# Performance work log

Measured on AMD Instinct MI355X. Metric: run time of the kernel, lower is better.

Reference implementation:

```python
import jax, jax.numpy as jnp
import numpy as np

EPS = 1e-3  # keras BatchNormalization default epsilon


def _dwconv_t(y, w):
    # depthwise conv along time (axis 1), SAME padding. y:(B,T,S,G,n), w:(G,n,k)
    k = w.shape[-1]
    T = y.shape[1]
    pl = (k - 1) // 2
    yp = jnp.pad(y, ((0, 0), (pl, k - 1 - pl), (0, 0), (0, 0), (0, 0)))
    return sum(yp[:, j:j + T] * w[..., j] for j in range(k))


def _tc_layer(x, w, b, k3, k5, k7, gamma, beta, mu, var):
    # x:(B,T,S,C); w:(5,G,Cg,nb); b/gamma/beta/mu/var:(5,G,nb); k*:(G,nb,k)
    B, T, S, C = x.shape
    G, nb = w.shape[1], w.shape[-1]
    # global spatial pooling: concat [x, max, mean] along spatial axis -> S+2
    x = jnp.concatenate([x, x.max(axis=2, keepdims=True), x.mean(axis=2, keepdims=True)], axis=2)
    S = S + 2
    xg = x.reshape(B, T, S, G, C // G)
    # 5 grouped 1x1x1 pointwise convs at once
    y = jnp.einsum('btsgc,pgcn->pbtsgn', xg, w) + b[:, None, None, None]
    t0 = y[0]
    t3 = _dwconv_t(y[1], k3)
    t5 = _dwconv_t(y[2], k5)
    t7 = _dwconv_t(y[3], k7)
    # temporal maxpool pool=2 stride=1 SAME (TF pads right)
    t1 = jnp.maximum(y[4], jnp.concatenate([y[4][:, 1:], y[4][:, -1:]], axis=1))
    ts = jnp.stack([t0, t3, t5, t7, t1])  # (5,B,T,S,G,nb)
    scale = gamma[:, None, None, None] / jnp.sqrt(var[:, None, None, None] + EPS)
    ts = (ts - mu[:, None, None, None]) * scale + beta[:, None, None, None]
    # concat branches within each group: (B,T,S,G,5*nb)
    z = jnp.transpose(ts, (1, 2, 3, 4, 0, 5)).reshape(B, T, S, G, 5 * nb)
    z = jax.nn.relu(z)
    # channel shuffle: (G, per) -> (per, G) -> flatten
    z = jnp.swapaxes(z, -1, -2).reshape(B, T, S, G * 5 * nb)
    # MaxPooling3D pool=(2,1,1) stride 2 valid: halve T
    return jnp.maximum(z[:, 0::2], z[:, 1::2])


def setup_inputs() -> dict:
    key = jax.random.key(0)
    ks = jax.random.split(key, 32)
    B, T, H, W, C = 16, 64, 7, 7, 1024
    G = 8
    d = {'x': jax.random.normal(ks[0], (B, T, H, W, C), jnp.float32)}
    specs = [(0, 128, 32), (1, 160, 40)]  # (layer, Cg, nb)
    i = 1
    for l, cg, nb in specs:
        d[f'w{l}'] = 0.02 * jax.random.normal(ks[i], (5, G, cg, nb)); i += 1
        d[f'b{l}'] = 0.02 * jax.random.normal(ks[i], (5, G, nb)); i += 1
        d[f'k3_{l}'] = 0.1 * jax.random.normal(ks[i], (G, nb, 3)); i += 1
        d[f'k5_{l}'] = 0.1 * jax.random.normal(ks[i], (G, nb, 5)); i += 1
        d[f'k7_{l}'] = 0.1 * jax.random.normal(ks[i], (G, nb, 7)); i += 1
        d[f'g{l}'] = jax.random.uniform(ks[i], (5, G, nb), minval=0.5, maxval=1.5); i += 1
        d[f'be{l}'] = 0.02 * jax.random.normal(ks[i], (5, G, nb)); i += 1
        d[f'mu{l}'] = 0.02 * jax.random.normal(ks[i], (5, G, nb)); i += 1
        d[f'v{l}'] = jax.random.uniform(ks[i], (5, G, nb), minval=0.5, maxval=1.5); i += 1
    return d


def reference(x, w0, b0, k3_0, k5_0, k7_0, g0, be0, mu0, v0,
              w1, b1, k3_1, k5_1, k7_1, g1, be1, mu1, v1):
    B, T, H, W, C = x.shape
    z = x.reshape(B, T, H * W, C)  # (B,T,S,C), side_dim2=1 kept implicit
    z = _tc_layer(z, w0, b0, k3_0, k5_0, k7_0, g0, be0, mu0, v0)
    z = _tc_layer(z, w1, b1, k3_1, k5_1, k7_1, g1, be1, mu1, v1)
    return z[:, :, :, None, :]  # (B, T/4, S+4, 1, Cout)
```

## Files before the change

### kernel.cpp

```cpp
#include <hip/hip_runtime.h>
#include <hip/hip_bf16.h>

#define EPSBN 1e-3f

typedef __attribute__((ext_vector_type(8))) short bf16x8;
typedef __attribute__((ext_vector_type(8))) unsigned short ushort8;
typedef __attribute__((ext_vector_type(4))) float f32x4;


__device__ __forceinline__ float bf2f(unsigned short u) {
    union { unsigned int i; float f; } c; c.i = (unsigned int)u << 16; return c.f;
}
__device__ __forceinline__ unsigned short f2bf(float f) {
    union { float f; unsigned int i; } c; c.f = f;
    unsigned int r = c.i + 0x7FFF + ((c.i >> 16) & 1);
    return (unsigned short)(r >> 16);
}

__global__ __launch_bounds__(256) void tc_prep(const float* __restrict__ w0,
                                               const float* __restrict__ w1,
                                               unsigned short* __restrict__ W0t,
                                               unsigned short* __restrict__ W1t) {
    const int idx = blockIdx.x * 256 + threadIdx.x;
    if (idx < 163840) {
        const int g   = idx / 20480;
        const int rem = idx - g*20480;
        const int n   = rem >> 7;
        const int k   = rem & 127;
        const int p   = n >> 5, nn = n & 31;
        W0t[idx] = f2bf(w0[(((size_t)p*8 + g)*128 + k)*32 + nn]);
    } else if (idx < 163840 + 256000) {
        const int i2  = idx - 163840;
        const int g   = i2 / 32000;
        const int rem = i2 - g*32000;
        const int n   = rem / 160;
        const int k   = rem - n*160;
        const int kref = (k % 20)*8 + k/20;
        const int p   = n / 40, nn = n - p*40;
        W1t[i2] = f2bf(w1[(((size_t)p*8 + g)*160 + kref)*40 + nn]);
    }
}

__global__ __launch_bounds__(256) void tc_reduce0(const float* __restrict__ x,
                                                  unsigned short* __restrict__ extb) {
    const int bt = blockIdx.x;
    const int b  = bt >> 6, t = bt & 63;
    const int c  = threadIdx.x * 4;
    const float4* src = reinterpret_cast<const float4*>(x + (size_t)bt * 49 * 1024 + c);
    float4 v = src[0];
    float mx0 = v.x, mx1 = v.y, mx2 = v.z, mx3 = v.w;
    float sm0 = v.x, sm1 = v.y, sm2 = v.z, sm3 = v.w;
    for (int s = 1; s < 49; ++s) {
        float4 u = src[(size_t)s * 256];
        mx0 = fmaxf(mx0, u.x); sm0 += u.x;
        mx1 = fmaxf(mx1, u.y); sm1 += u.y;
        mx2 = fmaxf(mx2, u.z); sm2 += u.z;
        mx3 = fmaxf(mx3, u.w); sm3 += u.w;
    }
    const float inv = 1.0f / 49.0f;
    ushort4 omx, omn;
    omx.x=f2bf(mx0); omx.y=f2bf(mx1); omx.z=f2bf(mx2); omx.w=f2bf(mx3);
    omn.x=f2bf(sm0*inv); omn.y=f2bf(sm1*inv); omn.z=f2bf(sm2*inv); omn.w=f2bf(sm3*inv);
    *reinterpret_cast<ushort4*>(&extb[((size_t)(b*2 + 0)*64 + t)*1024 + c]) = omx;
    *reinterpret_cast<ushort4*>(&extb[((size_t)(b*2 + 1)*64 + t)*1024 + c]) = omn;
}

__global__ __launch_bounds__(512, 4) void tc_layer0(
    const float* __restrict__ x, const unsigned short* __restrict__ extb,
    const unsigned short* __restrict__ W0t, const float* __restrict__ bias,
    const float* __restrict__ k3, const float* __restrict__ k5,
    const float* __restrict__ k7,
    const float* __restrict__ gam, const float* __restrict__ bet,
    const float* __restrict__ mu, const float* __restrict__ var,
    unsigned short* __restrict__ zb)
{
    const int tid = threadIdx.x;
    const int g   = blockIdx.x / 416;
    const int rem = blockIdx.x % 416;
    const int sp  = rem % 26;
    const int b   = rem / 26;
    const int s0  = sp*2;
    const int has1 = (s0 + 1 < 51);

    __shared__ __align__(16) unsigned short lds[128*136 + 160*40];
    unsigned short* AtU = lds;
    unsigned short* WtU = lds + 128*136;
    unsigned short* Ytb = lds;

    #pragma unroll
    for (int it = 0; it < 4; ++it) {
        const int fid = tid + it*512;
        const int row = fid >> 4;
        const int ch8 = (fid & 15) * 8;
        const int t   = row & 63;
        const int s   = (row < 64) ? s0 : (has1 ? s0+1 : s0);
        ushort8 u;
        if (s < 49) {
            const float* sp_ = x + ((size_t)(b*64 + t)*49 + s)*1024 + g*128 + ch8;
            const float4 f0 = *reinterpret_cast<const float4*>(sp_);
            const float4 f1 = *reinterpret_cast<const float4*>(sp_ + 4);
            u[0]=f2bf(f0.x); u[1]=f2bf(f0.y); u[2]=f2bf(f0.z); u[3]=f2bf(f0.w);
            u[4]=f2bf(f1.x); u[5]=f2bf(f1.y); u[6]=f2bf(f1.z); u[7]=f2bf(f1.w);
        } else {
            u = *reinterpret_cast<const ushort8*>(
                &extb[((size_t)(b*2 + (s-49))*64 + t)*1024 + g*128 + ch8]);
        }
        *reinterpret_cast<ushort8*>(&AtU[row*136 + ch8]) = u;
    }

    const int lane = tid & 63;
    const int wid  = tid >> 6;
    const int fr   = lane & 15;
    const int kb   = lane >> 4;

    f32x4 zero = {0.f, 0.f, 0.f, 0.f};
    f32x4 acc[10];
    #pragma unroll
    for (int i = 0; i < 10; ++i) acc[i] = zero;

    for (int kc = 0; kc < 4; ++kc) {
        __syncthreads();
        #pragma unroll
        for (int it = 0; it < 2; ++it) {
            const int gi = tid + it*512;
            if (gi < 640) {
                const int n = gi >> 2, part = (gi & 3) * 8;
                *reinterpret_cast<ushort8*>(&WtU[n*40 + part]) =
                    *reinterpret_cast<const ushort8*>(
                        &W0t[((size_t)g*160 + n)*128 + kc*32 + part]);
            }
        }
        __syncthreads();
        const bf16x8 bfrag = *reinterpret_cast<const bf16x8*>(
            &AtU[(wid*16 + fr)*136 + kc*32 + kb*8]);
        #pragma unroll
        for (int nt = 0; nt < 10; ++nt) {
            const bf16x8 afrag = *reinterpret_cast<const bf16x8*>(
                &WtU[(nt*16 + fr)*40 + kb*8]);
            acc[nt] = __builtin_amdgcn_mfma_f32_16x16x32_bf16(afrag, bfrag, acc[nt], 0, 0, 0);
        }
    }
    __syncthreads();
    #pragma unroll
    for (int nt = 0; nt < 10; ++nt)
        #pragma unroll
        for (int r = 0; r < 4; ++r)
            Ytb[(nt*16 + kb*4 + r)*134 + wid*16 + fr] = f2bf(acc[nt][r]);
    __syncthreads();

    if (tid < 320) {
        const int sIdx = (tid >= 160) ? 1 : 0;
        const int ch   = tid - sIdx*160;
        if (!sIdx || has1) {
            const int s  = s0 + sIdx;
            const int p  = ch >> 5, n = ch & 31;
            const int pi = (p*8 + g)*32 + n;
            const float bsv = bias[pi];
            const float sc  = gam[pi]*rsqrtf(var[pi]+EPSBN);
            const float sh  = bet[pi] - mu[pi]*sc;
            float yv[64];
            #pragma unroll
            for (int i = 0; i < 32; ++i) {
                const unsigned int w2 = *reinterpret_cast<const unsigned int*>(
                    &Ytb[ch*134 + sIdx*64 + i*2]);
                yv[2*i]   = bf2f((unsigned short)(w2 & 0xffffu)) + bsv;
                yv[2*i+1] = bf2f((unsigned short)(w2 >> 16)) + bsv;
            }
            unsigned short* zp = zb + ((size_t)(b*32)*53 + s)*1280 + g*160 + ch;
            if (p == 0) {
                #pragma unroll
                for (int tq = 0; tq < 32; ++tq) {
                    const float r = fmaxf(fmaxf(fmaf(yv[2*tq],sc,sh), fmaf(yv[2*tq+1],sc,sh)), 0.f);
                    zp[(size_t)tq*67840] = f2bf(r);
                }
            } else if (p == 1) {
                const float w0_ = k3[(g*32+n)*3+0], w1_ = k3[(g*32+n)*3+1], w2_ = k3[(g*32+n)*3+2];
                #pragma unroll
                for (int tq = 0; tq < 32; ++tq) {
                    float a = yv[2*tq]*w1_;
                    if (tq > 0) a = fmaf(yv[2*tq-1], w0_, a);
                    a = fmaf(yv[2*tq+1], w2_, a);
                    float c2 = fmaf(yv[2*tq], w0_, yv[2*tq+1]*w1_);
                    if (tq < 31) c2 = fmaf(yv[2*tq+2], w2_, c2);
                    const float r = fmaxf(fmaxf(fmaf(a,sc,sh), fmaf(c2,sc,sh)), 0.f);
                    zp[(size_t)tq*67840] = f2bf(r);
                }
            } else if (p == 2) {
                float wk[5];
                #pragma unroll
                for (int j = 0; j < 5; ++j) wk[j] = k5[(g*32+n)*5+j];
                #pragma unroll
                for (int tq = 0; tq < 32; ++tq) {
                    float vv[2];
                    #pragma unroll
                    for (int q = 0; q < 2; ++q) {
                        const int t = 2*tq + q;
                        float v = 0.f;
                        #pragma unroll
                        for (int j = 0; j < 5; ++j) {
                            const int ttp = t + j - 2;
                            if (ttp >= 0 && ttp < 64) v = fmaf(yv[ttp], wk[j], v);
                        }
                        vv[q] = v;
                    }
                    const float r = fmaxf(fmaxf(fmaf(vv[0],sc,sh), fmaf(vv[1],sc,sh)), 0.f);
                    zp[(size_t)tq*67840] = f2bf(r);
                }
            } else if (p == 3) {
                float wk[7];
                #pragma unroll
                for (int j = 0; j < 7; ++j) wk[j] = k7[(g*32+n)*7+j];
                #pragma unroll
                for (int tq = 0; tq < 32; ++tq) {
                    float vv[2];
                    #pragma unroll
                    for (int q = 0; q < 2; ++q) {
                        const int t = 2*tq + q;
                        float v = 0.f;
                        #pragma unroll
                        for (int j = 0; j < 7; ++j) {
                            const int ttp = t + j - 3;
                            if (ttp >= 0 && ttp < 64) v = fmaf(yv[ttp], wk[j], v);
                        }
                        vv[q] = v;
                    }
                    const float r = fmaxf(fmaxf(fmaf(vv[0],sc,sh), fmaf(vv[1],sc,sh)), 0.f);
                    zp[(size_t)tq*67840] = f2bf(r);
                }
            } else {
                #pragma unroll
                for (int tq = 0; tq < 32; ++tq) {
                    const float v0 = fmaxf(yv[2*tq], yv[2*tq+1]);
                    const float v1 = fmaxf(yv[2*tq+1], yv[(2*tq+2 < 64) ? 2*tq+2 : 63]);
                    const float r = fmaxf(fmaxf(fmaf(v0,sc,sh), fmaf(v1,sc,sh)), 0.f);
                    zp[(size_t)tq*67840] = f2bf(r);
                }
            }
        }
    }
}

__global__ __launch_bounds__(320) void tc_reduce1(unsigned short* __restrict__ zb) {
    const int bt = blockIdx.x;
    const int c  = threadIdx.x * 4;
    unsigned short* base = zb + (size_t)bt * 67840;
    ushort4 u = *reinterpret_cast<const ushort4*>(&base[c]);
    float v0 = bf2f(u.x), v1 = bf2f(u.y), v2 = bf2f(u.z), v3 = bf2f(u.w);
    float mx0 = v0, mx1 = v1, mx2 = v2, mx3 = v3;
    float sm0 = v0, sm1 = v1, sm2 = v2, sm3 = v3;
    for (int s = 1; s < 51; ++s) {
        ushort4 w = *reinterpret_cast<const ushort4*>(&base[(size_t)s*1280 + c]);
        v0 = bf2f(w.x); v1 = bf2f(w.y); v2 = bf2f(w.z); v3 = bf2f(w.w);
        mx0 = fmaxf(mx0, v0); sm0 += v0;
        mx1 = fmaxf(mx1, v1); sm1 += v1;
        mx2 = fmaxf(mx2, v2); sm2 += v2;
        mx3 = fmaxf(mx3, v3); sm3 += v3;
    }
    const float inv = 1.0f / 51.0f;
    ushort4 o;
    o.x = f2bf(mx0); o.y = f2bf(mx1); o.z = f2bf(mx2); o.w = f2bf(mx3);
    *reinterpret_cast<ushort4*>(&base[(size_t)51*1280 + c]) = o;
    o.x = f2bf(sm0*inv); o.y = f2bf(sm1*inv); o.z = f2bf(sm2*inv); o.w = f2bf(sm3*inv);
    *reinterpret_cast<ushort4*>(&base[(size_t)52*1280 + c]) = o;
}

__global__ __launch_bounds__(512, 4) void tc_layer1(
    const unsigned short* __restrict__ zbi,
    const unsigned short* __restrict__ W1t, const float* __restrict__ bias,
    const float* __restrict__ k3, const float* __restrict__ k5,
    const float* __restrict__ k7,
    const float* __restrict__ gam, const float* __restrict__ bet,
    const float* __restrict__ mu, const float* __restrict__ var,
    unsigned short* __restrict__ og)
{
    const int tid = threadIdx.x;
    const int g   = blockIdx.x / 224;
    const int rem = blockIdx.x % 224;
    const int sq  = rem % 14;
    const int b   = rem / 14;
    const int s0  = sq*4;
    const int ns  = (53 - s0 < 4) ? (53 - s0) : 4;

    __shared__ __align__(16) unsigned short lds[128*168 + 208*40];
    unsigned short* AtU = lds;
    unsigned short* WtU = lds + 128*168;
    unsigned short* Ytb = lds;

    if (tid < 40) {
        ushort8 z8 = {0,0,0,0,0,0,0,0};
        const int r = tid / 5, cp = tid - r*5;
        *reinterpret_cast<ushort8*>(&WtU[(200 + r)*40 + cp*8]) = z8;
    }

    #pragma unroll
    for (int it = 0; it < 10; ++it) {
        const int fid = tid + it*512;
        const int row = fid / 40;
        const int seg = fid - row*40;
        const int gg  = seg / 5, q = seg - gg*5;
        const int ch  = gg*160 + g*20 + q*4;
        const int sl  = row >> 5;
        const int s   = s0 + ((sl < ns) ? sl : 0);
        const int t   = row & 31;
        const unsigned short* src = zbi + ((size_t)(b*32 + t)*53 + s)*1280 + ch;
        *reinterpret_cast<ushort4*>(&AtU[row*168 + seg*4]) =
            *reinterpret_cast<const ushort4*>(src);
    }

    const int lane = tid & 63;
    const int wid  = tid >> 6;
    const int fr   = lane & 15;
    const int kb   = lane >> 4;

    f32x4 zero = {0.f, 0.f, 0.f, 0.f};
    f32x4 acc[13];
    #pragma unroll
    for (int i = 0; i < 13; ++i) acc[i] = zero;

    for (int kc = 0; kc < 5; ++kc) {
        __syncthreads();
        #pragma unroll
        for (int it = 0; it < 2; ++it) {
            const int gi = tid + it*512;
            if (gi < 800) {
                const int n = gi >> 2, part = (gi & 3) * 8;
                *reinterpret_cast<ushort8*>(&WtU[n*40 + part]) =
                    *reinterpret_cast<const ushort8*>(
                        &W1t[((size_t)g*200 + n)*160 + kc*32 + part]);
            }
        }
        __syncthreads();
        const bf16x8 bfrag = *reinterpret_cast<const bf16x8*>(
            &AtU[(wid*16 + fr)*168 + kc*32 + kb*8]);
        #pragma unroll
        for (int nt = 0; nt < 13; ++nt) {
            const bf16x8 afrag = *reinterpret_cast<const bf16x8*>(
                &WtU[(nt*16 + fr)*40 + kb*8]);
            acc[nt] = __builtin_amdgcn_mfma_f32_16x16x32_bf16(afrag, bfrag, acc[nt], 0, 0, 0);
        }
    }
    __syncthreads();
    #pragma unroll
    for (int nt = 0; nt < 13; ++nt) {
        #pragma unroll
        for (int r = 0; r < 4; ++r) {
            const int n = nt*16 + kb*4 + r;
            if (n < 200) Ytb[n*134 + wid*16 + fr] = f2bf(acc[nt][r]);
        }
    }
    __syncthreads();

    #pragma unroll
    for (int it = 0; it < 2; ++it) {
        const int task = tid + it*512;
        if (task < 800) {
            const int sIdx = task / 200;
            const int ch   = task - sIdx*200;
            if (sIdx < ns) {
                const int s  = s0 + sIdx;
                const int p  = ch / 40, n = ch - p*40;
                const int pi = (p*8 + g)*40 + n;
                const float bsv = bias[pi];
                const float sc  = gam[pi]*rsqrtf(var[pi]+EPSBN);
                const float sh  = bet[pi] - mu[pi]*sc;
                float yv[32];
                #pragma unroll
                for (int i = 0; i < 16; ++i) {
                    const unsigned int w2 = *reinterpret_cast<const unsigned int*>(
                        &Ytb[ch*134 + sIdx*32 + i*2]);
                    yv[2*i]   = bf2f((unsigned short)(w2 & 0xffffu)) + bsv;
                    yv[2*i+1] = bf2f((unsigned short)(w2 >> 16)) + bsv;
                }
                unsigned short* op = og + ((size_t)(b*16)*53 + s)*1600 + g*200 + ch;
                if (p == 0) {
                    #pragma unroll
                    for (int tq = 0; tq < 16; ++tq) {
                        const float r = fmaxf(fmaxf(fmaf(yv[2*tq],sc,sh), fmaf(yv[2*tq+1],sc,sh)), 0.f);
                        op[(size_t)tq*84800] = f2bf(r);
                    }
                } else if (p == 1) {
                    const float w0_ = k3[(g*40+n)*3+0], w1_ = k3[(g*40+n)*3+1], w2_ = k3[(g*40+n)*3+2];
                    #pragma unroll
                    for (int tq = 0; tq < 16; ++tq) {
                        float a = yv[2*tq]*w1_;
                        if (tq > 0) a = fmaf(yv[2*tq-1], w0_, a);
                        a = fmaf(yv[2*tq+1], w2_, a);
                        float c2 = fmaf(yv[2*tq], w0_, yv[2*tq+1]*w1_);
                        if (tq < 15) c2 = fmaf(yv[2*tq+2], w2_, c2);
                        const float r = fmaxf(fmaxf(fmaf(a,sc,sh), fmaf(c2,sc,sh)), 0.f);
                        op[(size_t)tq*84800] = f2bf(r);
                    }
                } else if (p == 2) {
                    float wk[5];
                    #pragma unroll
                    for (int j = 0; j < 5; ++j) wk[j] = k5[(g*40+n)*5+j];
                    #pragma unroll
                    for (int tq = 0; tq < 16; ++tq) {
                        float vv[2];
                        #pragma unroll
                        for (int q = 0; q < 2; ++q) {
                            const int t = 2*tq + q;
                            float v = 0.f;
                            #pragma unroll
                            for (int j = 0; j < 5; ++j) {
                                const int ttp = t + j - 2;
                                if (ttp >= 0 && ttp < 32) v = fmaf(yv[ttp], wk[j], v);
                            }
                            vv[q] = v;
                        }
                        const float r = fmaxf(fmaxf(fmaf(vv[0],sc,sh), fmaf(vv[1],sc,sh)), 0.f);
                        op[(size_t)tq*84800] = f2bf(r);
                    }
                } else if (p == 3) {
                    float wk[7];
                    #pragma unroll
                    for (int j = 0; j < 7; ++j) wk[j] = k7[(g*40+n)*7+j];
                    #pragma unroll
                    for (int tq = 0; tq < 16; ++tq) {
                        float vv[2];
                        #pragma unroll
                        for (int q = 0; q < 2; ++q) {
                            const int t = 2*tq + q;
                            float v = 0.f;
                            #pragma unroll
                            for (int j = 0; j < 7; ++j) {
                                const int ttp = t + j - 3;
                                if (ttp >= 0 && ttp < 32) v = fmaf(yv[ttp], wk[j], v);
                            }
                            vv[q] = v;
                        }
                        const float r = fmaxf(fmaxf(fmaf(vv[0],sc,sh), fmaf(vv[1],sc,sh)), 0.f);
                        op[(size_t)tq*84800] = f2bf(r);
                    }
                } else {
                    #pragma unroll
                    for (int tq = 0; tq < 16; ++tq) {
                        const float v0 = fmaxf(yv[2*tq], yv[2*tq+1]);
                        const float v1 = fmaxf(yv[2*tq+1], yv[(2*tq+2 < 32) ? 2*tq+2 : 31]);
                        const float r = fmaxf(fmaxf(fmaf(v0,sc,sh), fmaf(v1,sc,sh)), 0.f);
                        op[(size_t)tq*84800] = f2bf(r);
                    }
                }
            }
        }
    }
}

__global__ __launch_bounds__(256) void tc_shuffle(const unsigned short* __restrict__ og,
                                                  float* __restrict__ o) {
    __shared__ unsigned short row[1600];
    const size_t base = (size_t)blockIdx.x * 1600;
    const int tid = threadIdx.x;
    if (tid < 200)
        *reinterpret_cast<ushort8*>(&row[tid*8]) =
            *reinterpret_cast<const ushort8*>(&og[base + (size_t)tid*8]);
    __syncthreads();
    #pragma unroll
    for (int it = 0; it < 2; ++it) {
        const int f4 = tid + it*256;
        if (f4 < 400) {
            const int c = f4*4;
            float4 v;
            v.x = bf2f(row[((c  ) & 7)*200 + ((c  ) >> 3)]);
            v.y = bf2f(row[((c+1) & 7)*200 + ((c+1) >> 3)]);
            v.z = bf2f(row[((c+2) & 7)*200 + ((c+2) >> 3)]);
            v.w = bf2f(row[((c+3) & 7)*200 + ((c+3) >> 3)]);
            *reinterpret_cast<float4*>(&o[base + (size_t)c]) = v;
        }
    }
}

extern "C" void kernel_launch(void* const* d_in, const int* in_sizes, int n_in,
                              void* d_out, int out_size, void* d_ws, size_t ws_size,
                              hipStream_t stream) {
    const float* x    = (const float*)d_in[0];
    const float* w0   = (const float*)d_in[1];
    const float* b0   = (const float*)d_in[2];
    const float* k3_0 = (const float*)d_in[3];
    const float* k5_0 = (const float*)d_in[4];
    const float* k7_0 = (const float*)d_in[5];
    const float* g0   = (const float*)d_in[6];
    const float* be0  = (const float*)d_in[7];
    const float* mu0  = (const float*)d_in[8];
    const float* v0   = (const float*)d_in[9];
    const float* w1   = (const float*)d_in[10];
    const float* b1   = (const float*)d_in[11];
    const float* k3_1 = (const float*)d_in[12];
    const float* k5_1 = (const float*)d_in[13];
    const float* k7_1 = (const float*)d_in[14];
    const float* g1   = (const float*)d_in[15];
    const float* be1  = (const float*)d_in[16];
    const float* mu1  = (const float*)d_in[17];
    const float* v1   = (const float*)d_in[18];

    const size_t n_zb   = 34734080;
    const size_t n_W0t  = 163840;
    const size_t n_W1t  = 256000;
    const size_t n_extb = 2097152;

    unsigned short* zb   = (unsigned short*)d_ws;
    unsigned short* W0t  = zb + n_zb;
    unsigned short* W1t  = W0t + n_W0t;
    unsigned short* extb = W1t + n_W1t;
    unsigned short* og   = extb + n_extb;

    tc_prep   <<<1640, 256, 0, stream>>>(w0, w1, W0t, W1t);
    tc_reduce0<<<16*64, 256, 0, stream>>>(x, extb);
    tc_layer0 <<<416*8, 512, 0, stream>>>(x, extb, W0t, b0, k3_0, k5_0,
                                          k7_0, g0, be0, mu0, v0, zb);
    tc_reduce1<<<16*32, 320, 0, stream>>>(zb);
    tc_layer1 <<<224*8, 512, 0, stream>>>(zb, W1t, b1, k3_1, k5_1, k7_1,
                                          g1, be1, mu1, v1, og);
    tc_shuffle<<<16*16*53, 256, 0, stream>>>(og, (float*)d_out);
}
```

Before: 256.2 us.

## Merge prep/reduce kernels and split layer0 epilogue across more threads

Fuses the weight-prep and spatial-reduce kernels into one launch, removing a kernel launch and letting both run concurrently. In tc_layer0 the epilogue now splits each channel's time axis into two halves with a halo, so 640 tasks use all 512 threads instead of 320, and the conv branches share one generic loop with a sliding register window of 40 values instead of 64. Launch bounds are raised to 6 waves per SIMD to increase occupancy, which may force register spills. The halo loads add some redundant LDS reads, and the generic loop adds a runtime kernel-length check.

```diff
diff --git a/kernel.cpp b/kernel.cpp
--- a/kernel.cpp
+++ b/kernel.cpp
@@ -17,55 +17,55 @@
     return (unsigned short)(r >> 16);
 }
 
-__global__ __launch_bounds__(256) void tc_prep(const float* __restrict__ w0,
-                                               const float* __restrict__ w1,
-                                               unsigned short* __restrict__ W0t,
-                                               unsigned short* __restrict__ W1t) {
-    const int idx = blockIdx.x * 256 + threadIdx.x;
-    if (idx < 163840) {
-        const int g   = idx / 20480;
-        const int rem = idx - g*20480;
-        const int n   = rem >> 7;
-        const int k   = rem & 127;
-        const int p   = n >> 5, nn = n & 31;
-        W0t[idx] = f2bf(w0[(((size_t)p*8 + g)*128 + k)*32 + nn]);
-    } else if (idx < 163840 + 256000) {
-        const int i2  = idx - 163840;
-        const int g   = i2 / 32000;
-        const int rem = i2 - g*32000;
-        const int n   = rem / 160;
-        const int k   = rem - n*160;
-        const int kref = (k % 20)*8 + k/20;
-        const int p   = n / 40, nn = n - p*40;
-        W1t[i2] = f2bf(w1[(((size_t)p*8 + g)*160 + kref)*40 + nn]);
-    }
-}
-
-__global__ __launch_bounds__(256) void tc_reduce0(const float* __restrict__ x,
-                                                  unsigned short* __restrict__ extb) {
-    const int bt = blockIdx.x;
-    const int b  = bt >> 6, t = bt & 63;
-    const int c  = threadIdx.x * 4;
-    const float4* src = reinterpret_cast<const float4*>(x + (size_t)bt * 49 * 1024 + c);
-    float4 v = src[0];
-    float mx0 = v.x, mx1 = v.y, mx2 = v.z, mx3 = v.w;
-    float sm0 = v.x, sm1 = v.y, sm2 = v.z, sm3 = v.w;
-    for (int s = 1; s < 49; ++s) {
-        float4 u = src[(size_t)s * 256];
-        mx0 = fmaxf(mx0, u.x); sm0 += u.x;
-        mx1 = fmaxf(mx1, u.y); sm1 += u.y;
-        mx2 = fmaxf(mx2, u.z); sm2 += u.z;
-        mx3 = fmaxf(mx3, u.w); sm3 += u.w;
-    }
-    const float inv = 1.0f / 49.0f;
-    ushort4 omx, omn;
-    omx.x=f2bf(mx0); omx.y=f2bf(mx1); omx.z=f2bf(mx2); omx.w=f2bf(mx3);
-    omn.x=f2bf(sm0*inv); omn.y=f2bf(sm1*inv); omn.z=f2bf(sm2*inv); omn.w=f2bf(sm3*inv);
-    *reinterpret_cast<ushort4*>(&extb[((size_t)(b*2 + 0)*64 + t)*1024 + c]) = omx;
-    *reinterpret_cast<ushort4*>(&extb[((size_t)(b*2 + 1)*64 + t)*1024 + c]) = omn;
-}
-
-__global__ __launch_bounds__(512, 4) void tc_layer0(
+__global__ __launch_bounds__(256) void tc_prep_reduce0(
+    const float* __restrict__ x, unsigned short* __restrict__ extb,
+    const float* __restrict__ w0, const float* __restrict__ w1,
+    unsigned short* __restrict__ W0t, unsigned short* __restrict__ W1t)
+{
+    if (blockIdx.x < 1024) {
+        const int bt = blockIdx.x;
+        const int b  = bt >> 6, t = bt & 63;
+        const int c  = threadIdx.x * 4;
+        const float4* src = reinterpret_cast<const float4*>(x + (size_t)bt * 49 * 1024 + c);
+        float4 v = src[0];
+        float mx0 = v.x, mx1 = v.y, mx2 = v.z, mx3 = v.w;
+        float sm0 = v.x, sm1 = v.y, sm2 = v.z, sm3 = v.w;
+        for (int s = 1; s < 49; ++s) {
+            float4 u = src[(size_t)s * 256];
+            mx0 = fmaxf(mx0, u.x); sm0 += u.x;
+            mx1 = fmaxf(mx1, u.y); sm1 += u.y;
+            mx2 = fmaxf(mx2, u.z); sm2 += u.z;
+            mx3 = fmaxf(mx3, u.w); sm3 += u.w;
+        }
+        const float inv = 1.0f / 49.0f;
+        ushort4 omx, omn;
+        omx.x=f2bf(mx0); omx.y=f2bf(mx1); omx.z=f2bf(mx2); omx.w=f2bf(mx3);
+        omn.x=f2bf(sm0*inv); omn.y=f2bf(sm1*inv); omn.z=f2bf(sm2*inv); omn.w=f2bf(sm3*inv);
+        *reinterpret_cast<ushort4*>(&extb[((size_t)(b*2 + 0)*64 + t)*1024 + c]) = omx;
+        *reinterpret_cast<ushort4*>(&extb[((size_t)(b*2 + 1)*64 + t)*1024 + c]) = omn;
+    } else {
+        const int idx = (blockIdx.x - 1024) * 256 + threadIdx.x;
+        if (idx < 163840) {
+            const int g   = idx / 20480;
+            const int rem = idx - g*20480;
+            const int n   = rem >> 7;
+            const int k   = rem & 127;
+            const int p   = n >> 5, nn = n & 31;
+            W0t[idx] = f2bf(w0[(((size_t)p*8 + g)*128 + k)*32 + nn]);
+        } else if (idx < 163840 + 256000) {
+            const int i2  = idx - 163840;
+            const int g   = i2 / 32000;
+            const int rem = i2 - g*32000;
+            const int n   = rem / 160;
+            const int k   = rem - n*160;
+            const int kref = (k % 20)*8 + k/20;
+            const int p   = n / 40, nn = n - p*40;
+            W1t[i2] = f2bf(w1[(((size_t)p*8 + g)*160 + kref)*40 + nn]);
+        }
+    }
+}
+
+__global__ __launch_bounds__(512, 6) void tc_layer0(
     const float* __restrict__ x, const unsigned short* __restrict__ extb,
     const unsigned short* __restrict__ W0t, const float* __restrict__ bias,
     const float* __restrict__ k3, const float* __restrict__ k5,
@@ -148,92 +148,85 @@
             Ytb[(nt*16 + kb*4 + r)*134 + wid*16 + fr] = f2bf(acc[nt][r]);
     __syncthreads();
 
-    if (tid < 320) {
-        const int sIdx = (tid >= 160) ? 1 : 0;
-        const int ch   = tid - sIdx*160;
-        if (!sIdx || has1) {
-            const int s  = s0 + sIdx;
-            const int p  = ch >> 5, n = ch & 31;
-            const int pi = (p*8 + g)*32 + n;
-            const float bsv = bias[pi];
-            const float sc  = gam[pi]*rsqrtf(var[pi]+EPSBN);
-            const float sh  = bet[pi] - mu[pi]*sc;
-            float yv[64];
-            #pragma unroll
-            for (int i = 0; i < 32; ++i) {
-                const unsigned int w2 = *reinterpret_cast<const unsigned int*>(
-                    &Ytb[ch*134 + sIdx*64 + i*2]);
-                yv[2*i]   = bf2f((unsigned short)(w2 & 0xffffu)) + bsv;
-                yv[2*i+1] = bf2f((unsigned short)(w2 >> 16)) + bsv;
-            }
-            unsigned short* zp = zb + ((size_t)(b*32)*53 + s)*1280 + g*160 + ch;
-            if (p == 0) {
+    #pragma unroll
+    for (int it2 = 0; it2 < 2; ++it2) {
+        const int task = tid + it2*512;
+        if (task < 640) {
+            const int ch   = task % 160;
+            const int rest = task / 160;
+            const int sIdx = rest >> 1;
+            const int th   = rest & 1;
+            if (!sIdx || has1) {
+                const int s  = s0 + sIdx;
+                const int p  = ch >> 5, n = ch & 31;
+                const int pi = (p*8 + g)*32 + n;
+                const float bsv = bias[pi];
+                const float sc  = gam[pi]*rsqrtf(var[pi]+EPSBN);
+                const float sh  = bet[pi] - mu[pi]*sc;
+                const int t0 = th*32 - 4;
+                float yw[40];
                 #pragma unroll
-                for (int tq = 0; tq < 32; ++tq) {
-                    const float r = fmaxf(fmaxf(fmaf(yv[2*tq],sc,sh), fmaf(yv[2*tq+1],sc,sh)), 0.f);
-                    zp[(size_t)tq*67840] = f2bf(r);
+                for (int i = 0; i < 40; i += 2) {
+                    const int t = t0 + i;
+                    if (t >= 0 && t < 64) {
+                        const unsigned int w2 = *reinterpret_cast<const unsigned int*>(
+                            &Ytb[ch*134 + sIdx*64 + t]);
+                        yw[i]   = bf2f((unsigned short)(w2 & 0xffffu)) + bsv;
+                        yw[i+1] = bf2f((unsigned short)(w2 >> 16)) + bsv;
+                    } else { yw[i] = 0.f; yw[i+1] = 0.f; }
                 }
-            } else if (p == 1) {
-                const float w0_ = k3[(g*32+n)*3+0], w1_ = k3[(g*32+n)*3+1], w2_ = k3[(g*32+n)*3+2];
-                #pragma unroll
-                for (int tq = 0; tq < 32; ++tq) {
-                    float a = yv[2*tq]*w1_;
-                    if (tq > 0) a = fmaf(yv[2*tq-1], w0_, a);
-                    a = fmaf(yv[2*tq+1], w2_, a);
-                    float c2 = fmaf(yv[2*tq], w0_, yv[2*tq+1]*w1_);
-                    if (tq < 31) c2 = fmaf(yv[2*tq+2], w2_, c2);
-                    const float r = fmaxf(fmaxf(fmaf(a,sc,sh), fmaf(c2,sc,sh)), 0.f);
-                    zp[(size_t)tq*67840] = f2bf(r);
-                }
-            } else if (p == 2) {
-                float wk[5];
-                #pragma unroll
-                for (int j = 0; j < 5; ++j) wk[j] = k5[(g*32+n)*5+j];
-                #pragma unroll
-                for (int tq = 0; tq < 32; ++tq) {
-                    float vv[2];
-                    #pragma unroll
-                    for (int q = 0; q < 2; ++q) {
-                        const int t = 2*tq + q;
-                        float v = 0.f;
+                unsigned short* zp = zb + ((size_t)(b*32)*53 + s)*1280 + g*160 + ch;
+                const int tqb = th*16;
+                if (p == 0) {
+                    #pragma unroll
+                    for (int q2 = 0; q2 < 16; ++q2) {
+                        const float r = fmaxf(fmaxf(fmaf(yw[2*q2+4],sc,sh),
+                                                    fmaf(yw[2*q2+5],sc,sh)), 0.f);
+                        zp[(size_t)(tqb+q2)*67840] = f2bf(r);
+                    }
+                } else if (p == 4) {
+                    #pragma unroll
+                    for (int q2 = 0; q2 < 16; ++q2) {
+                        const int tq = tqb + q2;
+                        const float v0 = fmaxf(yw[2*q2+4], yw[2*q2+5]);
+                        const float vb = (2*tq+2 < 64) ? yw[2*q2+6] : yw[35];
+                        const float v1 = fmaxf(yw[2*q2+5], vb);
+                        const float r = fmaxf(fmaxf(fmaf(v0,sc,sh), fmaf(v1,sc,sh)), 0.f);
+                        zp[(size_t)tq*67840] = f2bf(r);
+                    }
+                } else {
+                    float wk[7];
+                    int klen, off;
+                    if (p == 1) { klen = 3; off = 1;
                         #pragma unroll
-                        for (int j = 0; j < 5; ++j) {
-                            const int ttp = t + j - 2;
-                            if (ttp >= 0 && ttp < 64) v = fmaf(yv[ttp], wk[j], v);
+                        for (int j = 0; j < 3; ++j) wk[j] = k3[(g*32+n)*3+j];
+                    } else if (p == 2) { klen = 5; off = 2;
+                        #pragma unroll
+                        for (int j = 0; j < 5; ++j) wk[j] = k5[(g*32+n)*5+j];
+                    } else { klen = 7; off = 3;
+                        #pragma unroll
+                        for (int j = 0; j < 7; ++j) wk[j] = k7[(g*32+n)*7+j];
+                    }
+                    #pragma unroll
+                    for (int q2 = 0; q2 < 16; ++q2) {
+                        const int tq = tqb + q2;
+                        float vv[2];
+                        #pragma unroll
+                        for (int q = 0; q < 2; ++q) {
+                            const int t = 2*tq + q;
+                            float v = 0.f;
+                            for (int j = 0; j < 7; ++j) {
+                                if (j < klen) {
+                                    const int tt = t + j - off;
+                                    if (tt >= 0 && tt < 64)
+                                        v = fmaf(yw[2*q2 + 4 + q + j - off], wk[j], v);
+                                }
+                            }
+                            vv[q] = v;
                         }
-                        vv[q] = v;
-                    }
-                    const float r = fmaxf(fmaxf(fmaf(vv[0],sc,sh), fmaf(vv[1],sc,sh)), 0.f);
-                    zp[(size_t)tq*67840] = f2bf(r);
-                }
-            } else if (p == 3) {
-                float wk[7];
-                #pragma unroll
-                for (int j = 0; j < 7; ++j) wk[j] = k7[(g*32+n)*7+j];
-                #pragma unroll
-                for (int tq = 0; tq < 32; ++tq) {
-                    float vv[2];
-                    #pragma unroll
-                    for (int q = 0; q < 2; ++q) {
-                        const int t = 2*tq + q;
-                        float v = 0.f;
-                        #pragma unroll
-                        for (int j = 0; j < 7; ++j) {
-                            const int ttp = t + j - 3;
-                            if (ttp >= 0 && ttp < 64) v = fmaf(yv[ttp], wk[j], v);
-                        }
-                        vv[q] = v;
-                    }
-                    const float r = fmaxf(fmaxf(fmaf(vv[0],sc,sh), fmaf(vv[1],sc,sh)), 0.f);
-                    zp[(size_t)tq*67840] = f2bf(r);
-                }
-            } else {
-                #pragma unroll
-                for (int tq = 0; tq < 32; ++tq) {
-                    const float v0 = fmaxf(yv[2*tq], yv[2*tq+1]);
-                    const float v1 = fmaxf(yv[2*tq+1], yv[(2*tq+2 < 64) ? 2*tq+2 : 63]);
-                    const float r = fmaxf(fmaxf(fmaf(v0,sc,sh), fmaf(v1,sc,sh)), 0.f);
-                    zp[(size_t)tq*67840] = f2bf(r);
+                        const float r = fmaxf(fmaxf(fmaf(vv[0],sc,sh), fmaf(vv[1],sc,sh)), 0.f);
+                        zp[(size_t)tq*67840] = f2bf(r);
+                    }
                 }
             }
         }
@@ -504,8 +497,7 @@
     unsigned short* extb = W1t + n_W1t;
     unsigned short* og   = extb + n_extb;
 
-    tc_prep   <<<1640, 256, 0, stream>>>(w0, w1, W0t, W1t);
-    tc_reduce0<<<16*64, 256, 0, stream>>>(x, extb);
+    tc_prep_reduce0<<<1024 + 1640, 256, 0, stream>>>(x, extb, w0, w1, W0t, W1t);
     tc_layer0 <<<416*8, 512, 0, stream>>>(x, extb, W0t, b0, k3_0, k5_0,
                                           k7_0, g0, be0, mu0, v0, zb);
     tc_reduce1<<<16*32, 320, 0, stream>>>(zb);
```

New measurement: 528.7 us. 2.06x slower.
